# Performance work log

Hardware: AMD Instinct MI355X
Metric: run time of the kernel (lower is better)

The kernel has to match this reference:

```python
import jax, jax.numpy as jnp
import numpy as np

N = 100000
E = 1600000
H = 128


def setup_inputs() -> dict:
    key = jax.random.key(0)
    ks = jax.random.split(key, 9)
    s = 1.0 / np.sqrt(H)
    x = jax.random.normal(ks[0], (N, H), dtype=jnp.float32)
    edge_index = jax.random.randint(ks[1], (2, E), 0, N, dtype=jnp.int64)
    W1l = jax.random.uniform(ks[2], (H, H), jnp.float32, -s, s)
    b1l = jax.random.uniform(ks[3], (H,), jnp.float32, -s, s)
    W1r = jax.random.uniform(ks[4], (H, H), jnp.float32, -s, s)
    W2l = jax.random.uniform(ks[5], (H, H), jnp.float32, -s, s)
    b2l = jax.random.uniform(ks[6], (H,), jnp.float32, -s, s)
    W2r = jax.random.uniform(ks[7], (H, H), jnp.float32, -s, s)
    return {"x": x, "edge_index": edge_index, "W1l": W1l, "b1l": b1l,
            "W1r": W1r, "W2l": W2l, "b2l": b2l, "W2r": W2r}


def _sage(x, src, dst, Wl, bl, Wr):
    # mean-aggregate source features at destination nodes (PyG SAGEConv default)
    n = x.shape[0]
    msg = x[src]                                             # [E, H]
    summed = jax.ops.segment_sum(msg, dst, num_segments=n)   # [N, H]
    cnt = jax.ops.segment_sum(jnp.ones((src.shape[0],), x.dtype), dst,
                              num_segments=n)
    mean = summed / jnp.maximum(cnt, 1.0)[:, None]
    # out = lin_l(mean) + lin_r(x); bias only on lin_l
    return mean @ Wl.T + bl + x @ Wr.T


def reference(x, edge_index, W1l, b1l, W1r, W2l, b2l, W2r):
    src, dst = edge_index[0], edge_index[1]
    h1 = jax.nn.relu(_sage(x, src, dst, W1l, b1l, W1r))
    return _sage(h1, src, dst, W2l, b2l, W2r)
```

## Files before the change

### kernel.cpp

```cpp
#include <hip/hip_runtime.h>

#define N_NODES 100000
#define N_EDGES 1600000
#define H 128

#define NB 391
#define P1_EPB 4096
#define P1_BLOCKS ((N_EDGES + P1_EPB - 1) / P1_EPB)
#define P2_CAP 6144

typedef unsigned short u16;
typedef unsigned int u32;
typedef short bf16x8 __attribute__((ext_vector_type(8)));
typedef float f32x4 __attribute__((ext_vector_type(4)));

static __device__ __forceinline__ u16 f2bf(float f) {
    u32 u = __float_as_uint(f);
    u += 0x7fffu + ((u >> 16) & 1u);
    return (u16)(u >> 16);
}


__global__ void zero_ints(int* __restrict__ p, int n) {
    int i = blockIdx.x * blockDim.x + threadIdx.x;
    if (i < n) p[i] = 0;
}

__global__ __launch_bounds__(1024) void bucket_count(
    const int* __restrict__ dst, int* __restrict__ gcount)
{
    __shared__ int s_cnt[NB];
    const int t = threadIdx.x;
    const int e0 = blockIdx.x * P1_EPB;
    const int ecnt = min(P1_EPB, N_EDGES - e0);
    for (int i = t; i < NB; i += 1024) s_cnt[i] = 0;
    __syncthreads();
    for (int i = t; i < ecnt; i += 1024)
        atomicAdd(&s_cnt[dst[e0 + i] >> 8], 1);
    __syncthreads();
    for (int i = t; i < NB; i += 1024)
        if (s_cnt[i] > 0) atomicAdd(&gcount[i], s_cnt[i]);
}

__global__ __launch_bounds__(512) void bucket_scan(
    const int* __restrict__ gcount, int* __restrict__ bstart, int* __restrict__ bcur)
{
    __shared__ int s[512];
    int t = threadIdx.x;
    int v = (t < NB) ? gcount[t] : 0;
    s[t] = v;
    __syncthreads();
    for (int off = 1; off < 512; off <<= 1) {
        int add = (t >= off) ? s[t - off] : 0;
        __syncthreads();
        s[t] += add;
        __syncthreads();
    }
    if (t < NB) {
        int excl = s[t] - v;
        bstart[t] = excl;
        bcur[t] = excl;
    }
    if (t == NB - 1) bstart[NB] = s[t];
}

__global__ __launch_bounds__(1024) void p1_bin(
    const int* __restrict__ src, const int* __restrict__ dst,
    int* __restrict__ bcur, u32* __restrict__ csrp)
{
    __shared__ int s_cnt[NB];
    __shared__ int s_lstart[NB];
    __shared__ int s_gbase[NB];
    __shared__ int s_scan[512];
    __shared__ u32 s_val[P1_EPB];
    __shared__ u32 s_gaddr[P1_EPB];

    const int t = threadIdx.x;
    const int e0 = blockIdx.x * P1_EPB;
    const int ecnt = min(P1_EPB, N_EDGES - e0);

    for (int i = t; i < NB; i += 1024) s_cnt[i] = 0;
    __syncthreads();
    for (int i = t; i < ecnt; i += 1024)
        atomicAdd(&s_cnt[dst[e0 + i] >> 8], 1);
    __syncthreads();

    int v = (t < NB) ? s_cnt[t] : 0;
    if (t < 512) s_scan[t] = v;
    __syncthreads();
    for (int off = 1; off < 512; off <<= 1) {
        int add = (t < 512 && t >= off) ? s_scan[t - off] : 0;
        __syncthreads();
        if (t < 512) s_scan[t] += add;
        __syncthreads();
    }
    if (t < NB) {
        int ls = s_scan[t] - v;
        s_lstart[t] = ls;
        s_gbase[t] = (v > 0) ? atomicAdd(&bcur[t], v) : 0;
        s_cnt[t] = ls;
    }
    __syncthreads();

    for (int i = t; i < ecnt; i += 1024) {
        int d = dst[e0 + i];
        int s = src[e0 + i];
        int b = d >> 8;
        int slot = atomicAdd(&s_cnt[b], 1);
        s_val[slot]   = ((u32)(d & 255) << 17) | (u32)s;
        s_gaddr[slot] = (u32)(s_gbase[b] + (slot - s_lstart[b]));
    }
    __syncthreads();
    for (int i = t; i < ecnt; i += 1024)
        csrp[s_gaddr[i]] = s_val[i];
}

__global__ __launch_bounds__(1024) void p2_scatter(
    const int* __restrict__ bstart, int* __restrict__ rowstart,
    int* __restrict__ deg, int* __restrict__ csr)
{
    __shared__ u32 s_in[P2_CAP];
    __shared__ u32 s_out[P2_CAP];
    __shared__ int s_cnt[256];
    __shared__ int s_loc[256];
    const int b = blockIdx.x;
    const int t = threadIdx.x;
    const int n0 = b << 8;
    const int s0 = bstart[b];
    const int s1 = bstart[b + 1];
    const int cnt = s1 - s0;

    if (t < 256) s_cnt[t] = 0;
    __syncthreads();
    for (int i = t; i < cnt; i += 1024) {
        u32 p = (u32)csr[s0 + i];
        s_in[i] = p;
        atomicAdd(&s_cnt[p >> 17], 1);
    }
    __syncthreads();
    if (t < 256) s_loc[t] = s_cnt[t];
    __syncthreads();
    for (int off = 1; off < 256; off <<= 1) {
        int add = (t < 256 && t >= off) ? s_loc[t - off] : 0;
        __syncthreads();
        if (t < 256) s_loc[t] += add;
        __syncthreads();
    }
    if (t < 256) {
        int node = n0 + t;
        int excl = s_loc[t] - s_cnt[t];
        if (node < N_NODES) {
            rowstart[node] = s0 + excl;
            deg[node]      = s_cnt[t];
        }
        s_loc[t] = excl;
    }
    __syncthreads();
    for (int i = t; i < cnt; i += 1024) {
        u32 p = s_in[i];
        int pos = atomicAdd(&s_loc[p >> 17], 1);
        s_out[pos] = p & 0x1FFFFu;
    }
    __syncthreads();
    for (int i = t; i < cnt; i += 1024)
        csr[s0 + i] = (int)s_out[i];
}


__global__ __launch_bounds__(256) void cast_x(const float* __restrict__ in,
                                              u16* __restrict__ out) {
    int i = blockIdx.x * 256 + threadIdx.x;
    const float4 v0 = *(const float4*)(in + (size_t)i * 8);
    const float4 v1 = *(const float4*)(in + (size_t)i * 8 + 4);
    u16 o[8];
    o[0]=f2bf(v0.x); o[1]=f2bf(v0.y); o[2]=f2bf(v0.z); o[3]=f2bf(v0.w);
    o[4]=f2bf(v1.x); o[5]=f2bf(v1.y); o[6]=f2bf(v1.z); o[7]=f2bf(v1.w);
    *(bf16x8*)(out + (size_t)i * 8) = *(bf16x8*)o;
}

__global__ __launch_bounds__(256) void cast_w(const float* __restrict__ w1l,
                                              const float* __restrict__ w1r,
                                              const float* __restrict__ w2l,
                                              const float* __restrict__ w2r,
                                              u16* __restrict__ out) {
    int i = blockIdx.x * 256 + threadIdx.x;
    int mat = i >> 14, idx = i & 16383;
    const float* s = (mat == 0) ? w1l : (mat == 1) ? w1r : (mat == 2) ? w2l : w2r;
    out[i] = f2bf(s[idx]);
}

__global__ __launch_bounds__(256) void agg_bf16(
    const u16* __restrict__ xin, const int* __restrict__ csr,
    const int* __restrict__ rowstart, const int* __restrict__ deg,
    u16* __restrict__ mout)
{
    int w = (blockIdx.x * blockDim.x + threadIdx.x) >> 6;
    if (w >= N_NODES) return;
    int lane = threadIdx.x & 63;
    int beg = __builtin_amdgcn_readfirstlane(rowstart[w]);
    int d   = __builtin_amdgcn_readfirstlane(deg[w]);
    const u16* base = xin + (lane << 1);

    float ax[8], ay[8];
#pragma unroll
    for (int u = 0; u < 8; ++u) { ax[u] = 0.f; ay[u] = 0.f; }

    int i = 0;
    for (; i + 8 <= d; i += 8) {
        int s[8];
#pragma unroll
        for (int u = 0; u < 8; ++u) s[u] = csr[beg + i + u];
#pragma unroll
        for (int u = 0; u < 8; ++u) {
            u32 v = *(const u32*)(base + ((size_t)s[u] << 7));
            ax[u] += __uint_as_float(v << 16);
            ay[u] += __uint_as_float(v & 0xffff0000u);
        }
    }
    if (i < d) {
        int cnt = d - i;
        int s[8];
#pragma unroll
        for (int u = 0; u < 8; ++u) s[u] = csr[beg + i + ((u < cnt) ? u : 0)];
#pragma unroll
        for (int u = 0; u < 8; ++u) {
            u32 v = *(const u32*)(base + ((size_t)s[u] << 7));
            if (u < cnt) {
                ax[u] += __uint_as_float(v << 16);
                ay[u] += __uint_as_float(v & 0xffff0000u);
            }
        }
    }

#pragma unroll
    for (int u = 0; u < 4; ++u) { ax[u] += ax[u + 4]; ay[u] += ay[u + 4]; }
    ax[0] += ax[2]; ay[0] += ay[2];
    ax[1] += ax[3]; ay[1] += ay[3];
    ax[0] += ax[1]; ay[0] += ay[1];

    float inv = 1.f / (float)(d > 0 ? d : 1);
    u32 packed = (u32)f2bf(ax[0] * inv) | ((u32)f2bf(ay[0] * inv) << 16);
    *(u32*)(mout + ((size_t)w << 7) + (lane << 1)) = packed;
}

__global__ __launch_bounds__(256) void gemm_mfma4(
    const u16* __restrict__ Ab, const u16* __restrict__ Xb,
    const u16* __restrict__ Wlb, const float* __restrict__ bl,
    const u16* __restrict__ Wrb, void* __restrict__ outp, int relu_bf16)
{
    __shared__ u16 lds[32768];
    const int t  = threadIdx.x;
    const int wv = t >> 6;
    const int l  = t & 63;
    const int lr = l & 15;
    const int lq = l >> 4;
    const int r0 = blockIdx.x * 128;

    bf16x8 bwl[2][4], bwr[2][4];
#pragma unroll
    for (int ct = 0; ct < 2; ++ct) {
        const u16* wl = Wlb + (size_t)(wv * 32 + ct * 16 + lr) * H + lq * 8;
        const u16* wr = Wrb + (size_t)(wv * 32 + ct * 16 + lr) * H + lq * 8;
#pragma unroll
        for (int k0 = 0; k0 < 4; ++k0) {
            bwl[ct][k0] = *(const bf16x8*)(wl + k0 * 32);
            bwr[ct][k0] = *(const bf16x8*)(wr + k0 * 32);
        }
    }
    float bv[2] = { bl[wv * 32 + lr], bl[wv * 32 + 16 + lr] };

    const char* ag = (const char*)(Ab + (size_t)r0 * H);
    const char* xg = (const char*)(Xb + (size_t)r0 * H);
#pragma unroll
    for (int c = 0; c < 8; ++c) {
        int boff = wv * 8192 + c * 1024;
        __builtin_amdgcn_global_load_lds(
            (const u32*)(ag + boff + (l << 4)), (u32*)&lds[boff >> 1], 16, 0, 0);
        __builtin_amdgcn_global_load_lds(
            (const u32*)(xg + boff + (l << 4)), (u32*)&lds[(32768 + boff) >> 1], 16, 0, 0);
    }
    __syncthreads();

    f32x4 acc[8][2];
#pragma unroll
    for (int rt = 0; rt < 8; ++rt) {
        bf16x8 af[4], xf[4];
#pragma unroll
        for (int k0 = 0; k0 < 4; ++k0) {
            int idx = (rt * 16 + lr) * 128 + k0 * 32 + lq * 8;
            af[k0] = *(const bf16x8*)&lds[idx];
            xf[k0] = *(const bf16x8*)&lds[16384 + idx];
        }
#pragma unroll
        for (int ct = 0; ct < 2; ++ct) {
            f32x4 a = (f32x4)0.f;
#pragma unroll
            for (int k0 = 0; k0 < 4; ++k0) {
                a = __builtin_amdgcn_mfma_f32_16x16x32_bf16(af[k0], bwl[ct][k0], a, 0, 0, 0);
                a = __builtin_amdgcn_mfma_f32_16x16x32_bf16(xf[k0], bwr[ct][k0], a, 0, 0, 0);
            }
            acc[rt][ct] = a;
        }
    }
    __syncthreads();

    if (relu_bf16) {
#pragma unroll
        for (int rt = 0; rt < 8; ++rt)
#pragma unroll
        for (int ct = 0; ct < 2; ++ct)
#pragma unroll
        for (int r = 0; r < 4; ++r)
            lds[(rt * 16 + lq * 4 + r) * 128 + wv * 32 + ct * 16 + lr] =
                f2bf(fmaxf(acc[rt][ct][r] + bv[ct], 0.f));
        __syncthreads();
        u16* ob = (u16*)outp;
#pragma unroll
        for (int c = 0; c < 8; ++c) {
            int eoff = c * 2048 + t * 8;
            int row = r0 + (eoff >> 7);
            if (row < N_NODES)
                *(bf16x8*)(ob + (size_t)r0 * H + eoff) = *(const bf16x8*)&lds[eoff];
        }
    } else {
        float* of = (float*)lds;
#pragma unroll
        for (int rt = 0; rt < 8; ++rt)
#pragma unroll
        for (int ct = 0; ct < 2; ++ct)
#pragma unroll
        for (int r = 0; r < 4; ++r)
            of[(rt * 16 + lq * 4 + r) * 128 + wv * 32 + ct * 16 + lr] =
                acc[rt][ct][r] + bv[ct];
        __syncthreads();
        float* og = (float*)outp;
#pragma unroll
        for (int c = 0; c < 16; ++c) {
            int eoff = c * 1024 + t * 4;
            int row = r0 + (eoff >> 7);
            if (row < N_NODES)
                *(float4*)(og + (size_t)r0 * H + eoff) = *(const float4*)&of[eoff];
        }
    }
}


extern "C" void kernel_launch(void* const* d_in, const int* in_sizes, int n_in,
                              void* d_out, int out_size, void* d_ws, size_t ws_size,
                              hipStream_t stream) {
    const float* x   = (const float*)d_in[0];
    const int*   ei  = (const int*)d_in[1];
    const float* W1l = (const float*)d_in[2];
    const float* b1l = (const float*)d_in[3];
    const float* W1r = (const float*)d_in[4];
    const float* W2l = (const float*)d_in[5];
    const float* b2l = (const float*)d_in[6];
    const float* W2r = (const float*)d_in[7];

    const int* src = ei;
    const int* dst = ei + N_EDGES;

    u16* xb       = (u16*)d_ws;
    u16* mb       = xb + (size_t)N_NODES * H;
    int* deg      = (int*)(mb + (size_t)N_NODES * H);
    int* rowstart = deg + N_NODES;
    int* wslot    = rowstart + N_NODES;
    int* csr      = wslot + N_NODES;
    int* gcount   = csr + N_EDGES;
    int* bstart   = gcount + NB;
    int* bcur     = bstart + NB + 1;
    u16* Wb       = (u16*)wslot;
    u16* W1lb = Wb;
    u16* W1rb = Wb + 16384;
    u16* W2lb = Wb + 32768;
    u16* W2rb = Wb + 49152;

    zero_ints<<<(NB + 255) / 256, 256, 0, stream>>>(gcount, NB);
    bucket_count<<<P1_BLOCKS, 1024, 0, stream>>>(dst, gcount);
    bucket_scan<<<1, 512, 0, stream>>>(gcount, bstart, bcur);
    p1_bin<<<P1_BLOCKS, 1024, 0, stream>>>(src, dst, bcur, (u32*)csr);
    p2_scatter<<<NB, 1024, 0, stream>>>(bstart, rowstart, deg, csr);

    cast_w<<<65536 / 256, 256, 0, stream>>>(W1l, W1r, W2l, W2r, Wb);
    cast_x<<<(N_NODES * H / 8) / 256, 256, 0, stream>>>(x, xb);

    const int gemm_grid = (N_NODES + 127) / 128;

    agg_bf16<<<(N_NODES + 3) / 4, 256, 0, stream>>>(xb, csr, rowstart, deg, mb);
    gemm_mfma4<<<gemm_grid, 256, 0, stream>>>(mb, xb, W1lb, b1l, W1rb, xb, 1);

    agg_bf16<<<(N_NODES + 3) / 4, 256, 0, stream>>>(xb, csr, rowstart, deg, mb);
    gemm_mfma4<<<gemm_grid, 256, 0, stream>>>(mb, xb, W2lb, b2l, W2rb, d_out, 0);
}
```

Measured before the change: 240.3 us.

## Bin edges into fixed-capacity per-bucket staging, dropping the separate count pass

The separate bucket_count pass over all destination indices is removed. p1_bin now writes edges into a staging buffer with a fixed capacity (P2_CAP) per bucket, aliased onto the mb workspace, and obtains per-bucket offsets by atomics on bcur starting from zero. A scan over the final bucket counts then produces bstart, and p2_scatter reads each bucket's contiguous staging region to build the CSR. This saves one full read of dst and one kernel launch. The cost is a hard assumption that no 256-node bucket holds more than P2_CAP edges, which is safe only for near-uniform degree distributions.

```diff
diff --git a/kernel.cpp b/kernel.cpp
--- a/kernel.cpp
+++ b/kernel.cpp
@@ -26,47 +26,9 @@
     if (i < n) p[i] = 0;
 }
 
-__global__ __launch_bounds__(1024) void bucket_count(
-    const int* __restrict__ dst, int* __restrict__ gcount)
-{
-    __shared__ int s_cnt[NB];
-    const int t = threadIdx.x;
-    const int e0 = blockIdx.x * P1_EPB;
-    const int ecnt = min(P1_EPB, N_EDGES - e0);
-    for (int i = t; i < NB; i += 1024) s_cnt[i] = 0;
-    __syncthreads();
-    for (int i = t; i < ecnt; i += 1024)
-        atomicAdd(&s_cnt[dst[e0 + i] >> 8], 1);
-    __syncthreads();
-    for (int i = t; i < NB; i += 1024)
-        if (s_cnt[i] > 0) atomicAdd(&gcount[i], s_cnt[i]);
-}
-
-__global__ __launch_bounds__(512) void bucket_scan(
-    const int* __restrict__ gcount, int* __restrict__ bstart, int* __restrict__ bcur)
-{
-    __shared__ int s[512];
-    int t = threadIdx.x;
-    int v = (t < NB) ? gcount[t] : 0;
-    s[t] = v;
-    __syncthreads();
-    for (int off = 1; off < 512; off <<= 1) {
-        int add = (t >= off) ? s[t - off] : 0;
-        __syncthreads();
-        s[t] += add;
-        __syncthreads();
-    }
-    if (t < NB) {
-        int excl = s[t] - v;
-        bstart[t] = excl;
-        bcur[t] = excl;
-    }
-    if (t == NB - 1) bstart[NB] = s[t];
-}
-
 __global__ __launch_bounds__(1024) void p1_bin(
     const int* __restrict__ src, const int* __restrict__ dst,
-    int* __restrict__ bcur, u32* __restrict__ csrp)
+    int* __restrict__ bcur, u32* __restrict__ stage)
 {
     __shared__ int s_cnt[NB];
     __shared__ int s_lstart[NB];
@@ -108,16 +70,34 @@
         int b = d >> 8;
         int slot = atomicAdd(&s_cnt[b], 1);
         s_val[slot]   = ((u32)(d & 255) << 17) | (u32)s;
-        s_gaddr[slot] = (u32)(s_gbase[b] + (slot - s_lstart[b]));
+        s_gaddr[slot] = (u32)(b * P2_CAP + s_gbase[b] + (slot - s_lstart[b]));
     }
     __syncthreads();
     for (int i = t; i < ecnt; i += 1024)
-        csrp[s_gaddr[i]] = s_val[i];
+        stage[s_gaddr[i]] = s_val[i];
+}
+
+__global__ __launch_bounds__(512) void bucket_scan(
+    const int* __restrict__ bcur, int* __restrict__ bstart)
+{
+    __shared__ int s[512];
+    int t = threadIdx.x;
+    int v = (t < NB) ? bcur[t] : 0;
+    s[t] = v;
+    __syncthreads();
+    for (int off = 1; off < 512; off <<= 1) {
+        int add = (t >= off) ? s[t - off] : 0;
+        __syncthreads();
+        s[t] += add;
+        __syncthreads();
+    }
+    if (t < NB) bstart[t] = s[t] - v;
+    if (t == NB - 1) bstart[NB] = s[t];
 }
 
 __global__ __launch_bounds__(1024) void p2_scatter(
-    const int* __restrict__ bstart, int* __restrict__ rowstart,
-    int* __restrict__ deg, int* __restrict__ csr)
+    const int* __restrict__ bstart, const u32* __restrict__ stage,
+    int* __restrict__ rowstart, int* __restrict__ deg, int* __restrict__ csr)
 {
     __shared__ u32 s_in[P2_CAP];
     __shared__ u32 s_out[P2_CAP];
@@ -127,13 +107,13 @@
     const int t = threadIdx.x;
     const int n0 = b << 8;
     const int s0 = bstart[b];
-    const int s1 = bstart[b + 1];
-    const int cnt = s1 - s0;
+    const int cnt = bstart[b + 1] - s0;
+    const u32* sb = stage + (size_t)b * P2_CAP;
 
     if (t < 256) s_cnt[t] = 0;
     __syncthreads();
     for (int i = t; i < cnt; i += 1024) {
-        u32 p = (u32)csr[s0 + i];
+        u32 p = sb[i];
         s_in[i] = p;
         atomicAdd(&s_cnt[p >> 17], 1);
     }
@@ -366,20 +346,19 @@
     int* rowstart = deg + N_NODES;
     int* wslot    = rowstart + N_NODES;
     int* csr      = wslot + N_NODES;
-    int* gcount   = csr + N_EDGES;
-    int* bstart   = gcount + NB;
+    int* bstart   = csr + N_EDGES;
     int* bcur     = bstart + NB + 1;
+    u32* stage    = (u32*)mb;
     u16* Wb       = (u16*)wslot;
     u16* W1lb = Wb;
     u16* W1rb = Wb + 16384;
     u16* W2lb = Wb + 32768;
     u16* W2rb = Wb + 49152;
 
-    zero_ints<<<(NB + 255) / 256, 256, 0, stream>>>(gcount, NB);
-    bucket_count<<<P1_BLOCKS, 1024, 0, stream>>>(dst, gcount);
-    bucket_scan<<<1, 512, 0, stream>>>(gcount, bstart, bcur);
-    p1_bin<<<P1_BLOCKS, 1024, 0, stream>>>(src, dst, bcur, (u32*)csr);
-    p2_scatter<<<NB, 1024, 0, stream>>>(bstart, rowstart, deg, csr);
+    zero_ints<<<(NB + 255) / 256, 256, 0, stream>>>(bcur, NB);
+    p1_bin<<<P1_BLOCKS, 1024, 0, stream>>>(src, dst, bcur, stage);
+    bucket_scan<<<1, 512, 0, stream>>>(bcur, bstart);
+    p2_scatter<<<NB, 1024, 0, stream>>>(bstart, stage, rowstart, deg, csr);
 
     cast_w<<<65536 / 256, 256, 0, stream>>>(W1l, W1r, W2l, W2r, Wb);
     cast_x<<<(N_NODES * H / 8) / 256, 256, 0, stream>>>(x, xb);
```

Result: faster. 230.6 us (-4.0%).
